# Kernel tuning notes

Hardware: AMD Instinct MI355X
Metric: run time of the kernel (lower is better)

The kernel has to match this reference:

```python
import jax, jax.numpy as jnp
import numpy as np

N = 50000      # nodes
E = 800000     # edges (before self-loops)
IN = 256       # in_channels
HID = 128      # hidden_channels
OUT = 128      # out_channels
NEG_SLOPE = 0.2
EPS = 1e-16


def setup_inputs() -> dict:
    key = jax.random.key(0)
    ks = jax.random.split(key, 16)
    p = lambda k, shape: jax.random.normal(k, shape, jnp.float32) * 0.1
    return {
        "x": jax.random.normal(ks[0], (N, IN), jnp.float32),
        "edge_index": jax.random.randint(ks[1], (2, E), 0, N, dtype=jnp.int64),
        # semantic MLP
        "W1": p(ks[2], (IN, HID)), "b1": jnp.zeros((HID,), jnp.float32),
        "W2": p(ks[3], (HID, HID)), "b2": jnp.zeros((HID,), jnp.float32),
        # gat1: HID -> HID//2, heads=4, concat -> 2*HID
        "g1_W": p(ks[4], (HID, 4 * (HID // 2))),
        "g1_as": p(ks[5], (4, HID // 2)), "g1_ad": p(ks[6], (4, HID // 2)),
        "g1_b": jnp.zeros((4 * (HID // 2),), jnp.float32),
        # gat2: 2*HID -> OUT, heads=2, mean -> OUT
        "g2_W": p(ks[7], (2 * HID, 2 * OUT)),
        "g2_as": p(ks[8], (2, OUT)), "g2_ad": p(ks[9], (2, OUT)),
        "g2_b": jnp.zeros((OUT,), jnp.float32),
        # gat3: OUT -> OUT, heads=1, mean -> OUT
        "g3_W": p(ks[10], (OUT, OUT)),
        "g3_as": p(ks[11], (1, OUT)), "g3_ad": p(ks[12], (1, OUT)),
        "g3_b": jnp.zeros((OUT,), jnp.float32),
    }


def _gat(h_in, src, dst, W, a_src, a_dst, bias, heads, concat, n):
    # Linear projection into heads: [n, H, C]
    h = (h_in @ W).reshape(n, heads, -1)
    alpha_s = jnp.sum(h * a_src[None], axis=-1)  # [n, H]
    alpha_d = jnp.sum(h * a_dst[None], axis=-1)  # [n, H]
    e = jax.nn.leaky_relu(alpha_s[src] + alpha_d[dst], NEG_SLOPE)  # [E', H]
    # segment softmax over edges grouped by destination node
    m = jax.ops.segment_max(e, dst, num_segments=n)
    ex = jnp.exp(e - m[dst])
    denom = jax.ops.segment_sum(ex, dst, num_segments=n)
    alpha = ex / (denom[dst] + EPS)  # [E', H]
    msg = h[src] * alpha[..., None]  # [E', H, C]
    out = jax.ops.segment_sum(msg, dst, num_segments=n)  # [n, H, C]
    out = out.reshape(n, -1) if concat else out.mean(axis=1)
    return out + bias


def reference(x, edge_index, W1, b1, W2, b2,
              g1_W, g1_as, g1_ad, g1_b,
              g2_W, g2_as, g2_ad, g2_b,
              g3_W, g3_as, g3_ad, g3_b):
    n = x.shape[0]
    # PyG GATConv add_self_loops=True: append self-loop edges once
    loops = jnp.arange(n, dtype=edge_index.dtype)
    src = jnp.concatenate([edge_index[0], loops])
    dst = jnp.concatenate([edge_index[1], loops])
    # semantic MLP (inference: dropout = identity)
    h = jax.nn.relu(x @ W1 + b1)
    h = jax.nn.relu(h @ W2 + b2)
    h = jax.nn.elu(_gat(h, src, dst, g1_W, g1_as, g1_ad, g1_b, 4, True, n))
    h = jax.nn.elu(_gat(h, src, dst, g2_W, g2_as, g2_ad, g2_b, 2, False, n))
    h = _gat(h, src, dst, g3_W, g3_as, g3_ad, g3_b, 1, False, n)
    return h
```

## Files before the change

kernel.cpp:

```cpp
#include <hip/hip_runtime.h>
#include <math.h>


#define NEG_SLOPE 0.2f
#define EPS_DEN 1e-16f

typedef __attribute__((ext_vector_type(8))) short short8;
typedef __attribute__((ext_vector_type(4))) float f32x4;
typedef __attribute__((ext_vector_type(2))) float f32x2;
typedef __attribute__((ext_vector_type(4))) unsigned short u16x4;

__device__ inline unsigned short f2b(float f) {
  unsigned u = __builtin_bit_cast(unsigned, f);
  unsigned r = (u + 0x7fffu + ((u >> 16) & 1u)) >> 16;
  return (unsigned short)r;
}
__device__ inline float b2f(unsigned short u) {
  return __builtin_bit_cast(float, (unsigned)u << 16);
}

__device__ inline void glds16(const void* g, void* l) {
  __builtin_amdgcn_global_load_lds(
      (const __attribute__((address_space(1))) void*)g,
      (__attribute__((address_space(3))) void*)l, 16, 0, 0);
}

__device__ inline f32x2 pk_fma(f32x2 a, f32x2 b, f32x2 c) {
  f32x2 d;
  asm("v_pk_fma_f32 %0, %1, %2, %3" : "=v"(d) : "v"(a), "v"(b), "v"(c));
  return d;
}

__device__ inline void accum8(f32x2 acc2[4], const short8 r, float w) {
  const f32x2 wv = {w, w};
  const unsigned* u = (const unsigned*)&r;
#pragma unroll
  for (int p = 0; p < 4; p++) {
    const unsigned lo = u[p] << 16;
    const unsigned hi = u[p] & 0xffff0000u;
    f32x2 val = {__builtin_bit_cast(float, lo), __builtin_bit_cast(float, hi)};
    acc2[p] = pk_fma(val, wv, acc2[p]);
  }
}

template <int H>
__device__ inline void loadH(const float* p, float* v) {
  if constexpr (H == 4) {
    float4 t = *(const float4*)p;
    v[0] = t.x; v[1] = t.y; v[2] = t.z; v[3] = t.w;
  } else if constexpr (H == 2) {
    float2 t = *(const float2*)p;
    v[0] = t.x; v[1] = t.y;
  } else {
    v[0] = *p;
  }
}

template <int ACT, int OBF, int H, int CC>
__global__ __launch_bounds__(256) void mfma_gemm(
    const unsigned short* __restrict__ A, const unsigned short* __restrict__ Bt,
    const float* __restrict__ bias, float* __restrict__ Cf,
    unsigned short* __restrict__ Cb, const float* __restrict__ a_s,
    const float* __restrict__ a_d, float* __restrict__ alS,
    float* __restrict__ alD, int n, int K, int M) {
  __shared__ unsigned short As[64 * 64];
  __shared__ unsigned short Bs[128 * 64];

  const int tid = threadIdx.x;
  const int w = tid >> 6, lane = tid & 63;
  const int row0 = blockIdx.x * 64, col0 = blockIdx.y * 128;
  const int lr = lane >> 3, lg = lane & 7;
  const int lm = lane & 15, kg = lane >> 4;
  const int wm = (w >> 1) * 32, wn = (w & 1) * 64;

  f32x4 acc[2][4];
#pragma unroll
  for (int i = 0; i < 2; i++)
#pragma unroll
    for (int j = 0; j < 4; j++) acc[i][j] = {0.f, 0.f, 0.f, 0.f};

  const int swz = (lg ^ lr) << 3;

  for (int k0 = 0; k0 < K; k0 += 64) {
    __syncthreads();
#pragma unroll
    for (int it = 0; it < 2; it++) {
      const int r = w * 16 + it * 8;
      glds16(A + (size_t)(row0 + r + lr) * K + k0 + swz, &As[r * 64]);
    }
#pragma unroll
    for (int it = 0; it < 4; it++) {
      const int r = w * 32 + it * 8;
      glds16(Bt + (size_t)(col0 + r + lr) * K + k0 + swz, &Bs[r * 64]);
    }
    __syncthreads();

#pragma unroll
    for (int kh = 0; kh < 2; kh++) {
      const int sw = ((kh * 4 + kg) ^ (lm & 7)) << 3;
      short8 aF[2], bF[4];
#pragma unroll
      for (int i = 0; i < 2; i++)
        aF[i] = *(const short8*)&As[(wm + i * 16 + lm) * 64 + sw];
#pragma unroll
      for (int j = 0; j < 4; j++)
        bF[j] = *(const short8*)&Bs[(wn + j * 16 + lm) * 64 + sw];
#pragma unroll
      for (int i = 0; i < 2; i++)
#pragma unroll
        for (int j = 0; j < 4; j++)
          acc[i][j] = __builtin_amdgcn_mfma_f32_16x16x32_bf16(
              aF[i], bF[j], acc[i][j], 0, 0, 0);
    }
  }

  const int r4 = kg * 4;

  if constexpr (H > 0) {
    const int head = (col0 + wn) / CC;
    const int ch0 = (col0 + wn) % CC;
    float asv[4], adv[4];
#pragma unroll
    for (int j = 0; j < 4; j++) {
      asv[j] = a_s[head * CC + ch0 + j * 16 + lm];
      adv[j] = a_d[head * CC + ch0 + j * 16 + lm];
    }
    float psA[2][4], pdA[2][4];
#pragma unroll
    for (int i = 0; i < 2; i++) {
#pragma unroll
      for (int r = 0; r < 4; r++) {
        float ps = 0.f, pd = 0.f;
#pragma unroll
        for (int j = 0; j < 4; j++) {
          ps += acc[i][j][r] * asv[j];
          pd += acc[i][j][r] * adv[j];
        }
#pragma unroll
        for (int off = 1; off < 16; off <<= 1) {
          ps += __shfl_xor(ps, off, 64);
          pd += __shfl_xor(pd, off, 64);
        }
        psA[i][r] = ps;
        pdA[i][r] = pd;
      }
    }
    if constexpr (CC == 64) {
      if (lm == 0) {
#pragma unroll
        for (int i = 0; i < 2; i++)
#pragma unroll
          for (int r = 0; r < 4; r++) {
            const int row = row0 + wm + i * 16 + r4 + r;
            if (row < n) {
              alS[(size_t)row * H + head] = psA[i][r];
              alD[(size_t)row * H + head] = pdA[i][r];
            }
          }
      }
    } else {
      __shared__ float redS[4][32];
      __shared__ float redD[4][32];
      if (lm == 0) {
#pragma unroll
        for (int i = 0; i < 2; i++)
#pragma unroll
          for (int r = 0; r < 4; r++) {
            redS[w][i * 16 + r4 + r] = psA[i][r];
            redD[w][i * 16 + r4 + r] = pdA[i][r];
          }
      }
      __syncthreads();
      if ((w & 1) == 0 && lane < 32) {
        const int row = row0 + wm + lane;
        if (row < n) {
          const int hd = col0 / CC;
          alS[(size_t)row * H + hd] = redS[w][lane] + redS[w + 1][lane];
          alD[(size_t)row * H + hd] = redD[w][lane] + redD[w + 1][lane];
        }
      }
    }
  }

#pragma unroll
  for (int j = 0; j < 4; j++) {
    const int col = col0 + wn + j * 16 + lm;
    const float bv = bias ? bias[col] : 0.f;
#pragma unroll
    for (int i = 0; i < 2; i++) {
#pragma unroll
      for (int r = 0; r < 4; r++) {
        const int row = row0 + wm + i * 16 + r4 + r;
        if (row < n) {
          float v = acc[i][j][r] + bv;
          if (ACT == 1) v = v > 0.f ? v : 0.f;
          if (OBF)
            Cb[(size_t)row * M + col] = f2b(v);
          else
            Cf[(size_t)row * M + col] = v;
        }
      }
    }
  }
}

__global__ __launch_bounds__(256) void mlp_g1_kernel(
    const unsigned short* __restrict__ X, const unsigned short* __restrict__ W1t,
    const float* __restrict__ b1, const unsigned short* __restrict__ W2t,
    const float* __restrict__ b2, const unsigned short* __restrict__ G1Wt,
    const float* __restrict__ a_s, const float* __restrict__ a_d,
    float* __restrict__ alS, float* __restrict__ alD,
    unsigned short* __restrict__ Pb,
    const int* __restrict__ esrc, const int* __restrict__ edst,
    const int* __restrict__ rank, const int* __restrict__ rowptr,
    int* __restrict__ csr_src, int E, int n) {
  __shared__ unsigned short As[64 * 64];
  __shared__ unsigned short Bs[128 * 64];
  __shared__ unsigned short H1s[64 * 136];

  const int tid = threadIdx.x;
  const int w = tid >> 6, lane = tid & 63;
  const int row0 = blockIdx.x * 64;
  const int lr = lane >> 3, lg = lane & 7;
  const int lm = lane & 15, kg = lane >> 4;
  const int wm = (w >> 1) * 32, wn = (w & 1) * 64;
  const int swz = (lg ^ lr) << 3;
  const int r4 = kg * 4;

  {
    const int tot = E + n;
    const int gsz = (int)gridDim.x * 256;
    for (int i = (int)blockIdx.x * 256 + tid; i < tot; i += gsz) {
      int s, d;
      if (i < E) {
        s = __builtin_nontemporal_load(esrc + i);
        d = __builtin_nontemporal_load(edst + i);
      } else {
        s = d = i - E;
      }
      if ((unsigned)d < (unsigned)n && (unsigned)s < (unsigned)n) {
        const int pos = rowptr[d] + __builtin_nontemporal_load(rank + i);
        __builtin_nontemporal_store(s, csr_src + pos);
      }
    }
  }

  f32x4 acc[2][4];
#pragma unroll
  for (int i = 0; i < 2; i++)
#pragma unroll
    for (int j = 0; j < 4; j++) acc[i][j] = {0.f, 0.f, 0.f, 0.f};

  for (int k0 = 0; k0 < 256; k0 += 64) {
    __syncthreads();
#pragma unroll
    for (int it = 0; it < 2; it++) {
      const int r = w * 16 + it * 8;
      glds16(X + (size_t)(row0 + r + lr) * 256 + k0 + swz, &As[r * 64]);
    }
#pragma unroll
    for (int it = 0; it < 4; it++) {
      const int r = w * 32 + it * 8;
      glds16(W1t + (size_t)(r + lr) * 256 + k0 + swz, &Bs[r * 64]);
    }
    __syncthreads();
#pragma unroll
    for (int kh = 0; kh < 2; kh++) {
      const int sw = ((kh * 4 + kg) ^ (lm & 7)) << 3;
      short8 aF[2], bF[4];
#pragma unroll
      for (int i = 0; i < 2; i++)
        aF[i] = *(const short8*)&As[(wm + i * 16 + lm) * 64 + sw];
#pragma unroll
      for (int j = 0; j < 4; j++)
        bF[j] = *(const short8*)&Bs[(wn + j * 16 + lm) * 64 + sw];
#pragma unroll
      for (int i = 0; i < 2; i++)
#pragma unroll
        for (int j = 0; j < 4; j++)
          acc[i][j] = __builtin_amdgcn_mfma_f32_16x16x32_bf16(
              aF[i], bF[j], acc[i][j], 0, 0, 0);
    }
  }

#pragma unroll
  for (int j = 0; j < 4; j++) {
    const int col = wn + j * 16 + lm;
    const float bv = b1[col];
#pragma unroll
    for (int i = 0; i < 2; i++) {
#pragma unroll
      for (int r = 0; r < 4; r++) {
        const int lrow = wm + i * 16 + r4 + r;
        float v = acc[i][j][r] + bv;
        v = v > 0.f ? v : 0.f;
        H1s[lrow * 136 + col] = f2b(v);
      }
    }
  }
#pragma unroll
  for (int i = 0; i < 2; i++)
#pragma unroll
    for (int j = 0; j < 4; j++) acc[i][j] = {0.f, 0.f, 0.f, 0.f};
  __syncthreads();

  for (int k0 = 0; k0 < 128; k0 += 64) {
    __syncthreads();
#pragma unroll
    for (int it = 0; it < 4; it++) {
      const int r = w * 32 + it * 8;
      glds16(W2t + (size_t)(r + lr) * 128 + k0 + swz, &Bs[r * 64]);
    }
    __syncthreads();
#pragma unroll
    for (int kh = 0; kh < 2; kh++) {
      const int swB = ((kh * 4 + kg) ^ (lm & 7)) << 3;
      const int kofs = k0 + (kh * 4 + kg) * 8;
      short8 aF[2], bF[4];
#pragma unroll
      for (int i = 0; i < 2; i++)
        aF[i] = *(const short8*)&H1s[(wm + i * 16 + lm) * 136 + kofs];
#pragma unroll
      for (int j = 0; j < 4; j++)
        bF[j] = *(const short8*)&Bs[(wn + j * 16 + lm) * 64 + swB];
#pragma unroll
      for (int i = 0; i < 2; i++)
#pragma unroll
        for (int j = 0; j < 4; j++)
          acc[i][j] = __builtin_amdgcn_mfma_f32_16x16x32_bf16(
              aF[i], bF[j], acc[i][j], 0, 0, 0);
    }
  }

  __syncthreads();
#pragma unroll
  for (int j = 0; j < 4; j++) {
    const int col = wn + j * 16 + lm;
    const float bv = b2[col];
#pragma unroll
    for (int i = 0; i < 2; i++) {
#pragma unroll
      for (int r = 0; r < 4; r++) {
        const int lrow = wm + i * 16 + r4 + r;
        float v = acc[i][j][r] + bv;
        v = v > 0.f ? v : 0.f;
        H1s[lrow * 136 + col] = f2b(v);
      }
    }
  }
  __syncthreads();

  for (int c = 0; c < 2; c++) {
#pragma unroll
    for (int i = 0; i < 2; i++)
#pragma unroll
      for (int j = 0; j < 4; j++) acc[i][j] = {0.f, 0.f, 0.f, 0.f};

    for (int k0 = 0; k0 < 128; k0 += 64) {
      __syncthreads();
#pragma unroll
      for (int it = 0; it < 4; it++) {
        const int r = w * 32 + it * 8;
        glds16(G1Wt + (size_t)(c * 128 + r + lr) * 128 + k0 + swz,
               &Bs[r * 64]);
      }
      __syncthreads();
#pragma unroll
      for (int kh = 0; kh < 2; kh++) {
        const int swB = ((kh * 4 + kg) ^ (lm & 7)) << 3;
        const int kofs = k0 + (kh * 4 + kg) * 8;
        short8 aF[2], bF[4];
#pragma unroll
        for (int i = 0; i < 2; i++)
          aF[i] = *(const short8*)&H1s[(wm + i * 16 + lm) * 136 + kofs];
#pragma unroll
        for (int j = 0; j < 4; j++)
          bF[j] = *(const short8*)&Bs[(wn + j * 16 + lm) * 64 + swB];
#pragma unroll
        for (int i = 0; i < 2; i++)
#pragma unroll
          for (int j = 0; j < 4; j++)
            acc[i][j] = __builtin_amdgcn_mfma_f32_16x16x32_bf16(
                aF[i], bF[j], acc[i][j], 0, 0, 0);
      }
    }

    {
      const int head = c * 2 + (wn >> 6);
      float asv[4], adv[4];
#pragma unroll
      for (int j = 0; j < 4; j++) {
        asv[j] = a_s[head * 64 + j * 16 + lm];
        adv[j] = a_d[head * 64 + j * 16 + lm];
      }
#pragma unroll
      for (int i = 0; i < 2; i++) {
#pragma unroll
        for (int r = 0; r < 4; r++) {
          float ps = 0.f, pd = 0.f;
#pragma unroll
          for (int j = 0; j < 4; j++) {
            ps += acc[i][j][r] * asv[j];
            pd += acc[i][j][r] * adv[j];
          }
#pragma unroll
          for (int off = 1; off < 16; off <<= 1) {
            ps += __shfl_xor(ps, off, 64);
            pd += __shfl_xor(pd, off, 64);
          }
          if (lm == 0) {
            const int row = row0 + wm + i * 16 + r4 + r;
            if (row < n) {
              alS[(size_t)row * 4 + head] = ps;
              alD[(size_t)row * 4 + head] = pd;
            }
          }
        }
      }
    }

#pragma unroll
    for (int j = 0; j < 4; j++) {
      const int col = c * 128 + wn + j * 16 + lm;
#pragma unroll
      for (int i = 0; i < 2; i++) {
#pragma unroll
        for (int r = 0; r < 4; r++) {
          const int row = row0 + wm + i * 16 + r4 + r;
          if (row < n) Pb[(size_t)row * 256 + col] = f2b(acc[i][j][r]);
        }
      }
    }
  }
}

struct PrepArgs {
  const float* x; unsigned short* xb; long long nx;
  const float* W[5]; unsigned short* Wt[5];
  int K[5], M[5], t0[6];
  int* deg; int* rank; const int* edst; int E; int N;
};

__global__ __launch_bounds__(256) void fused_prep_kernel(PrepArgs a) {
  const int tid = threadIdx.x, bid = blockIdx.x, nb = gridDim.x;
  const long long gt = (long long)bid * 256 + tid;
  const long long gsz = (long long)nb * 256;
  __shared__ float tt[32][33];

  const long long etot = (long long)a.E + a.N;
  for (long long i = gt; i < etot; i += gsz) {
    int d = (i < a.E) ? __builtin_nontemporal_load(a.edst + i)
                      : (int)(i - a.E);
    if ((unsigned)d < (unsigned)a.N)
      a.rank[i] = atomicAdd(&a.deg[d], 1);
  }
  for (long long i = gt * 4; i < a.nx; i += gsz * 4) {
    float4 v = *(const float4*)(a.x + i);
    u16x4 u = {f2b(v.x), f2b(v.y), f2b(v.z), f2b(v.w)};
    *(u16x4*)(a.xb + i) = u;
  }
  for (int t = bid; t < a.t0[5]; t += nb) {
    int di = 0;
    while (t >= a.t0[di + 1]) di++;
    const int local = t - a.t0[di];
    const int K = a.K[di], M = a.M[di], mtiles = M / 32;
    const int mb = (local % mtiles) * 32, kb = (local / mtiles) * 32;
    const float* W = a.W[di];
    unsigned short* Wt = a.Wt[di];
    const int tx = tid & 31, ty = tid >> 5;
    __syncthreads();
#pragma unroll
    for (int i = 0; i < 4; i++)
      tt[ty + i * 8][tx] = W[(size_t)(kb + ty + i * 8) * M + mb + tx];
    __syncthreads();
#pragma unroll
    for (int i = 0; i < 4; i++)
      Wt[(size_t)(mb + ty + i * 8) * K + kb + tx] = f2b(tt[tx][ty + i * 8]);
  }
}

__global__ __launch_bounds__(256) void block_reduce_kernel(
    const int* __restrict__ deg, int* __restrict__ bsum, int n) {
  __shared__ int s[256];
  const int t = threadIdx.x, i = blockIdx.x * 256 + t;
  s[t] = (i < n) ? deg[i] : 0;
  __syncthreads();
#pragma unroll
  for (int off = 128; off; off >>= 1) {
    if (t < off) s[t] += s[t + off];
    __syncthreads();
  }
  if (t == 0) bsum[blockIdx.x] = s[0];
}

__global__ __launch_bounds__(256) void scan_bsums_kernel(int* __restrict__ bsum,
                                                         int nb) {
  __shared__ int s[256];
  const int t = threadIdx.x;
  const int v = (t < nb) ? bsum[t] : 0;
  s[t] = v;
  __syncthreads();
#pragma unroll
  for (int off = 1; off < 256; off <<= 1) {
    int a = (t >= off) ? s[t - off] : 0;
    __syncthreads();
    s[t] += a;
    __syncthreads();
  }
  if (t < nb) bsum[t] = s[t] - v;
}

__global__ __launch_bounds__(256) void scan_final_kernel(
    const int* __restrict__ deg, const int* __restrict__ bsumx,
    int* __restrict__ rowptr, int n) {
  __shared__ int s[256];
  const int t = threadIdx.x, i = blockIdx.x * 256 + t;
  const int v = (i < n) ? deg[i] : 0;
  s[t] = v;
  __syncthreads();
#pragma unroll
  for (int off = 1; off < 256; off <<= 1) {
    int a = (t >= off) ? s[t - off] : 0;
    __syncthreads();
    s[t] += a;
    __syncthreads();
  }
  if (i < n) {
    const int base = bsumx[blockIdx.x];
    rowptr[i] = base + s[t] - v;
    if (i == n - 1) rowptr[n] = base + s[t];
  }
}

template <int H, int C, bool CONCAT, int ACT, int OBF>
__global__ __launch_bounds__(256) void gat_fused_kernel(
    const unsigned short* __restrict__ proj, const float* __restrict__ alpha_s,
    const float* __restrict__ alpha_d, const int* __restrict__ rowptr,
    const int* __restrict__ csr_src, const float* __restrict__ bias,
    void* __restrict__ out, int n) {
  constexpr int HC = H * C;
  constexpr int ROWSPAN = HC / 8;
  constexpr int EDGES = 64 / ROWSPAN;
  constexpr int WLANES = C / 8;

  __shared__ float exs[4][64 * H];
  __shared__ int sids[4][64];

  const int wv = threadIdx.x >> 6;
  const int wid = (blockIdx.x * blockDim.x + threadIdx.x) >> 6;
  const int lane = threadIdx.x & 63;
  if (wid >= n) return;
  const int dst = wid;
  const int eslot = lane / ROWSPAN;
  const int sl = lane % ROWSPAN;
  const int h_lane = (sl * 8) / C;
  float* myex = &exs[wv][0];
  int* mysid = &sids[wv][0];

  float adv[H];
  loadH<H>(alpha_d + (size_t)dst * H, adv);
  const int rs = rowptr[dst], re = rowptr[dst + 1];

  float denomp[H];
#pragma unroll
  for (int h = 0; h < H; h++) denomp[h] = 0.f;
  f32x2 acc2[4];
#pragma unroll
  for (int p = 0; p < 4; p++) acc2[p] = {0.f, 0.f};

  const unsigned short* prow = proj + sl * 8;

  for (int base = rs; base < re; base += 64) {
    const int cnt = min(64, re - base);
    if (lane < cnt) {
      const int s = __builtin_nontemporal_load(csr_src + base + lane);
      mysid[lane] = s;
      float as[H];
      loadH<H>(alpha_s + (size_t)s * H, as);
#pragma unroll
      for (int h = 0; h < H; h++) {
        float e = as[h] + adv[h];
        e = e > 0.f ? e : NEG_SLOPE * e;
        const float ex = __expf(e);
        denomp[h] += ex;
        myex[lane * H + h] = ex;
      }
    }
    __builtin_amdgcn_wave_barrier();
    int j = eslot;
    for (; j + EDGES < cnt; j += 2 * EDGES) {
      const int s0 = mysid[j];
      const int s1 = mysid[j + EDGES];
      const float w0 = myex[j * H + h_lane];
      const float w1 = myex[(j + EDGES) * H + h_lane];
      const short8 r0 = *(const short8*)(prow + (size_t)s0 * HC);
      const short8 r1 = *(const short8*)(prow + (size_t)s1 * HC);
      accum8(acc2, r0, w0);
      accum8(acc2, r1, w1);
    }
    for (; j < cnt; j += EDGES) {
      const int s0 = mysid[j];
      const float w0 = myex[j * H + h_lane];
      const short8 r0 = *(const short8*)(prow + (size_t)s0 * HC);
      accum8(acc2, r0, w0);
    }
    __builtin_amdgcn_wave_barrier();
  }

  float acc[8];
#pragma unroll
  for (int p = 0; p < 4; p++) {
    acc[2 * p] = acc2[p].x;
    acc[2 * p + 1] = acc2[p].y;
  }

#pragma unroll
  for (int off = 32; off; off >>= 1)
#pragma unroll
    for (int h = 0; h < H; h++)
      denomp[h] += __shfl_xor(denomp[h], off, 64);
#pragma unroll
  for (int off = ROWSPAN; off < 64; off <<= 1)
#pragma unroll
    for (int k = 0; k < 8; k++) acc[k] += __shfl_xor(acc[k], off, 64);

  const float inv = 1.f / (denomp[h_lane] + EPS_DEN);
  float v[8];
#pragma unroll
  for (int k = 0; k < 8; k++) v[k] = acc[k] * inv;

  if (!CONCAT && H == 2) {
#pragma unroll
    for (int k = 0; k < 8; k++) v[k] += __shfl_xor(v[k], 16, 64);
  }

  if (CONCAT) {
    if (eslot != 0) return;
    const int c0 = sl * 8;
    float vv[8];
#pragma unroll
    for (int k = 0; k < 8; k++) {
      float t = v[k] + bias[c0 + k];
      if (ACT == 1) t = t > 0.f ? t : (__expf(t) - 1.f);
      vv[k] = t;
    }
    if (OBF) {
      short8 o;
#pragma unroll
      for (int k = 0; k < 8; k++) o[k] = (short)f2b(vv[k]);
      __builtin_nontemporal_store(
          o, (short8*)((unsigned short*)out + (size_t)dst * HC + c0));
    } else {
      float* op = (float*)out + (size_t)dst * HC + c0;
      f32x4 o0 = {vv[0], vv[1], vv[2], vv[3]};
      f32x4 o1 = {vv[4], vv[5], vv[6], vv[7]};
      __builtin_nontemporal_store(o0, (f32x4*)op);
      __builtin_nontemporal_store(o1, (f32x4*)(op + 4));
    }
  } else {
    if (eslot != 0 || sl >= WLANES) return;
    const int c0 = sl * 8;
    const float invH = 1.f / (float)H;
    float vv[8];
#pragma unroll
    for (int k = 0; k < 8; k++) {
      float t = v[k] * invH + bias[c0 + k];
      if (ACT == 1) t = t > 0.f ? t : (__expf(t) - 1.f);
      vv[k] = t;
    }
    if (OBF) {
      short8 o;
#pragma unroll
      for (int k = 0; k < 8; k++) o[k] = (short)f2b(vv[k]);
      __builtin_nontemporal_store(
          o, (short8*)((unsigned short*)out + (size_t)dst * C + c0));
    } else {
      float* op = (float*)out + (size_t)dst * C + c0;
      f32x4 o0 = {vv[0], vv[1], vv[2], vv[3]};
      f32x4 o1 = {vv[4], vv[5], vv[6], vv[7]};
      __builtin_nontemporal_store(o0, (f32x4*)op);
      __builtin_nontemporal_store(o1, (f32x4*)(op + 4));
    }
  }
}

extern "C" void kernel_launch(void* const* d_in, const int* in_sizes, int n_in,
                              void* d_out, int out_size, void* d_ws,
                              size_t ws_size, hipStream_t stream) {
  const float* x    = (const float*)d_in[0];
  const int*   ei   = (const int*)d_in[1];
  const float* W1   = (const float*)d_in[2];
  const float* b1   = (const float*)d_in[3];
  const float* W2   = (const float*)d_in[4];
  const float* b2   = (const float*)d_in[5];
  const float* g1W  = (const float*)d_in[6];
  const float* g1as = (const float*)d_in[7];
  const float* g1ad = (const float*)d_in[8];
  const float* g1b  = (const float*)d_in[9];
  const float* g2W  = (const float*)d_in[10];
  const float* g2as = (const float*)d_in[11];
  const float* g2ad = (const float*)d_in[12];
  const float* g2b  = (const float*)d_in[13];
  const float* g3W  = (const float*)d_in[14];
  const float* g3as = (const float*)d_in[15];
  const float* g3ad = (const float*)d_in[16];
  const float* g3b  = (const float*)d_in[17];

  const int N = in_sizes[0] / 256;
  const int E = in_sizes[1] / 2;
  const int Etot = E + N;
  const int NT = (N + 127) / 128;
  const int NT64 = (N + 63) / 64;
  const int NP = NT * 128;
  const int NB = (N + 255) / 256;

  char* p = (char*)d_ws;
  unsigned short* Pb  = (unsigned short*)p; p += (size_t)NP * 256 * 2;
  unsigned short* xb  = (unsigned short*)p; p += (size_t)NP * 256 * 2;
  unsigned short* h2b = (unsigned short*)p; p += (size_t)NP * 128 * 2;
  unsigned short* W1t = (unsigned short*)p; p += (size_t)128 * 256 * 2;
  unsigned short* W2t = (unsigned short*)p; p += (size_t)128 * 128 * 2;
  unsigned short* g1Wt = (unsigned short*)p; p += (size_t)256 * 128 * 2;
  unsigned short* g2Wt = (unsigned short*)p; p += (size_t)256 * 256 * 2;
  unsigned short* g3Wt = (unsigned short*)p; p += (size_t)128 * 128 * 2;
  float* alB = (float*)p; p += (size_t)N * 14 * 4;
  float* alS1 = alB;
  float* alD1 = alB + (size_t)4 * N;
  float* alS2 = alB + (size_t)8 * N;
  float* alD2 = alB + (size_t)10 * N;
  float* alS3 = alB + (size_t)12 * N;
  float* alD3 = alB + (size_t)13 * N;
  int* deg    = (int*)p; p += (size_t)N * 4;
  int* rowptr = (int*)p; p += (size_t)(N + 1) * 4;
  int* bsum   = (int*)p; p += 256 * 4;
  int* rank   = (int*)p; p += (size_t)Etot * 4;
  int* csrsrc = (int*)p;

  const int* esrc = ei;
  const int* edst = ei + E;
  unsigned short* act1b = xb;
  unsigned short* act2b = h2b;

  hipMemsetAsync(deg, 0, (size_t)N * 4, stream);

  PrepArgs pa;
  pa.x = x; pa.xb = xb; pa.nx = (long long)N * 256;
  pa.W[0] = W1;  pa.Wt[0] = W1t;  pa.K[0] = 256; pa.M[0] = 128;
  pa.W[1] = W2;  pa.Wt[1] = W2t;  pa.K[1] = 128; pa.M[1] = 128;
  pa.W[2] = g1W; pa.Wt[2] = g1Wt; pa.K[2] = 128; pa.M[2] = 256;
  pa.W[3] = g2W; pa.Wt[3] = g2Wt; pa.K[3] = 256; pa.M[3] = 256;
  pa.W[4] = g3W; pa.Wt[4] = g3Wt; pa.K[4] = 128; pa.M[4] = 128;
  pa.t0[0] = 0;
  for (int i = 0; i < 5; i++)
    pa.t0[i + 1] = pa.t0[i] + (pa.K[i] / 32) * (pa.M[i] / 32);
  pa.deg = deg; pa.rank = rank; pa.edst = edst; pa.E = E; pa.N = N;
  fused_prep_kernel<<<2048, 256, 0, stream>>>(pa);

  block_reduce_kernel<<<NB, 256, 0, stream>>>(deg, bsum, N);
  scan_bsums_kernel<<<1, 256, 0, stream>>>(bsum, NB);
  scan_final_kernel<<<NB, 256, 0, stream>>>(deg, bsum, rowptr, N);

  mlp_g1_kernel<<<NT64, 256, 0, stream>>>(xb, W1t, b1, W2t, b2, g1Wt, g1as,
                                          g1ad, alS1, alD1, Pb, esrc, edst,
                                          rank, rowptr, csrsrc, E, N);

  gat_fused_kernel<4, 64, true, 1, 1><<<(N + 3) / 4, 256, 0, stream>>>(
      Pb, alS1, alD1, rowptr, csrsrc, g1b, act1b, N);

  mfma_gemm<0, 1, 2, 128><<<dim3(NT64, 2), 256, 0, stream>>>(
      act1b, g2Wt, nullptr, nullptr, Pb, g2as, g2ad, alS2, alD2, N, 256, 256);
  gat_fused_kernel<2, 128, false, 1, 1><<<(N + 3) / 4, 256, 0, stream>>>(
      Pb, alS2, alD2, rowptr, csrsrc, g2b, act2b, N);

  mfma_gemm<0, 1, 1, 128><<<dim3(NT64, 1), 256, 0, stream>>>(
      act2b, g3Wt, nullptr, nullptr, Pb, g3as, g3ad, alS3, alD3, N, 128, 128);
  gat_fused_kernel<1, 128, false, 0, 0><<<(N + 3) / 4, 256, 0, stream>>>(
      Pb, alS3, alD3, rowptr, csrsrc, g3b, d_out, N);
}
```

Baseline: 423.2 us.

## Build CSR degree counts with LDS-privatized per-chunk histograms instead of global atomics

Replaces the global atomicAdd degree counting in the prep kernel with a separate kernel that splits edges into 32 chunks and nodes into 16 ranges, counting in shared-memory histograms. Per-chunk counts are summed for degrees and turned into per-chunk prefix offsets that the CSR scatter adds to each edge's position. This targets contention on global atomics, at the cost of rereading the edge list once per node range, a 32×N histogram buffer, and an extra launch plus longer reduce and scan passes.

```diff
diff --git a/kernel.cpp b/kernel.cpp
--- a/kernel.cpp
+++ b/kernel.cpp
@@ -4,6 +4,8 @@
 
 #define NEG_SLOPE 0.2f
 #define EPS_DEN 1e-16f
+#define PR 16
+#define QC 32
 
 typedef __attribute__((ext_vector_type(8))) short short8;
 typedef __attribute__((ext_vector_type(4))) float f32x4;
@@ -213,7 +215,7 @@
     unsigned short* __restrict__ Pb,
     const int* __restrict__ esrc, const int* __restrict__ edst,
     const int* __restrict__ rank, const int* __restrict__ rowptr,
-    int* __restrict__ csr_src, int E, int n) {
+    const int* __restrict__ Cpref, int* __restrict__ csr_src, int E, int n) {
   __shared__ unsigned short As[64 * 64];
   __shared__ unsigned short Bs[128 * 64];
   __shared__ unsigned short H1s[64 * 136];
@@ -229,6 +231,7 @@
 
   {
     const int tot = E + n;
+    const int CS = (tot + QC - 1) / QC;
     const int gsz = (int)gridDim.x * 256;
     for (int i = (int)blockIdx.x * 256 + tid; i < tot; i += gsz) {
       int s, d;
@@ -239,7 +242,9 @@
         s = d = i - E;
       }
       if ((unsigned)d < (unsigned)n && (unsigned)s < (unsigned)n) {
-        const int pos = rowptr[d] + __builtin_nontemporal_load(rank + i);
+        const int q = i / CS;
+        const int pos = rowptr[d] + Cpref[(size_t)q * n + d] +
+                        __builtin_nontemporal_load(rank + i);
         __builtin_nontemporal_store(s, csr_src + pos);
       }
     }
@@ -438,7 +443,6 @@
   const float* x; unsigned short* xb; long long nx;
   const float* W[5]; unsigned short* Wt[5];
   int K[5], M[5], t0[6];
-  int* deg; int* rank; const int* edst; int E; int N;
 };
 
 __global__ __launch_bounds__(256) void fused_prep_kernel(PrepArgs a) {
@@ -447,13 +451,6 @@
   const long long gsz = (long long)nb * 256;
   __shared__ float tt[32][33];
 
-  const long long etot = (long long)a.E + a.N;
-  for (long long i = gt; i < etot; i += gsz) {
-    int d = (i < a.E) ? __builtin_nontemporal_load(a.edst + i)
-                      : (int)(i - a.E);
-    if ((unsigned)d < (unsigned)a.N)
-      a.rank[i] = atomicAdd(&a.deg[d], 1);
-  }
   for (long long i = gt * 4; i < a.nx; i += gsz * 4) {
     float4 v = *(const float4*)(a.x + i);
     u16x4 u = {f2b(v.x), f2b(v.y), f2b(v.z), f2b(v.w)};
@@ -479,11 +476,46 @@
   }
 }
 
+__global__ __launch_bounds__(256) void count_hist_kernel(
+    const int* __restrict__ edst, int* __restrict__ rank,
+    int* __restrict__ C, int E, int n) {
+  __shared__ int h[3200];
+  const int tid = threadIdx.x;
+  const int q = blockIdx.x, p = blockIdx.y;
+  const int RANGE = (n + PR - 1) / PR;
+  const int lo = p * RANGE;
+
+  for (int i = tid; i < RANGE; i += 256) h[i] = 0;
+  __syncthreads();
+
+  const int tot = E + n;
+  const int CS = (tot + QC - 1) / QC;
+  const int start = q * CS;
+  const int end = min(start + CS, tot);
+  for (int i = start + tid; i < end; i += 256) {
+    int d = (i < E) ? __builtin_nontemporal_load(edst + i) : (i - E);
+    const int r = d - lo;
+    if ((unsigned)r < (unsigned)RANGE && d < n)
+      __builtin_nontemporal_store(atomicAdd(&h[r], 1), rank + i);
+  }
+  __syncthreads();
+
+  for (int i = tid; i < RANGE; i += 256)
+    if (lo + i < n) C[(size_t)q * n + lo + i] = h[i];
+}
+
 __global__ __launch_bounds__(256) void block_reduce_kernel(
-    const int* __restrict__ deg, int* __restrict__ bsum, int n) {
+    const int* __restrict__ C, int* __restrict__ deg, int* __restrict__ bsum,
+    int n) {
   __shared__ int s[256];
   const int t = threadIdx.x, i = blockIdx.x * 256 + t;
-  s[t] = (i < n) ? deg[i] : 0;
+  int v = 0;
+  if (i < n) {
+#pragma unroll
+    for (int q = 0; q < QC; q++) v += C[(size_t)q * n + i];
+    deg[i] = v;
+  }
+  s[t] = v;
   __syncthreads();
 #pragma unroll
   for (int off = 128; off; off >>= 1) {
@@ -511,8 +543,8 @@
 }
 
 __global__ __launch_bounds__(256) void scan_final_kernel(
-    const int* __restrict__ deg, const int* __restrict__ bsumx,
-    int* __restrict__ rowptr, int n) {
+    const int* __restrict__ deg, int* __restrict__ C,
+    const int* __restrict__ bsumx, int* __restrict__ rowptr, int n) {
   __shared__ int s[256];
   const int t = threadIdx.x, i = blockIdx.x * 256 + t;
   const int v = (i < n) ? deg[i] : 0;
@@ -529,6 +561,13 @@
     const int base = bsumx[blockIdx.x];
     rowptr[i] = base + s[t] - v;
     if (i == n - 1) rowptr[n] = base + s[t];
+    int run = 0;
+#pragma unroll
+    for (int q = 0; q < QC; q++) {
+      const int c = C[(size_t)q * n + i];
+      C[(size_t)q * n + i] = run;
+      run += c;
+    }
   }
 }
 
@@ -734,6 +773,7 @@
   int* rowptr = (int*)p; p += (size_t)(N + 1) * 4;
   int* bsum   = (int*)p; p += 256 * 4;
   int* rank   = (int*)p; p += (size_t)Etot * 4;
+  int* Chist  = (int*)p; p += (size_t)QC * N * 4;
   int* csrsrc = (int*)p;
 
   const int* esrc = ei;
@@ -741,7 +781,7 @@
   unsigned short* act1b = xb;
   unsigned short* act2b = h2b;
 
-  hipMemsetAsync(deg, 0, (size_t)N * 4, stream);
+  count_hist_kernel<<<dim3(QC, PR), 256, 0, stream>>>(edst, rank, Chist, E, N);
 
   PrepArgs pa;
   pa.x = x; pa.xb = xb; pa.nx = (long long)N * 256;
@@ -753,16 +793,15 @@
   pa.t0[0] = 0;
   for (int i = 0; i < 5; i++)
     pa.t0[i + 1] = pa.t0[i] + (pa.K[i] / 32) * (pa.M[i] / 32);
-  pa.deg = deg; pa.rank = rank; pa.edst = edst; pa.E = E; pa.N = N;
   fused_prep_kernel<<<2048, 256, 0, stream>>>(pa);
 
-  block_reduce_kernel<<<NB, 256, 0, stream>>>(deg, bsum, N);
+  block_reduce_kernel<<<NB, 256, 0, stream>>>(Chist, deg, bsum, N);
   scan_bsums_kernel<<<1, 256, 0, stream>>>(bsum, NB);
-  scan_final_kernel<<<NB, 256, 0, stream>>>(deg, bsum, rowptr, N);
+  scan_final_kernel<<<NB, 256, 0, stream>>>(deg, Chist, bsum, rowptr, N);
 
   mlp_g1_kernel<<<NT64, 256, 0, stream>>>(xb, W1t, b1, W2t, b2, g1Wt, g1as,
                                           g1ad, alS1, alD1, Pb, esrc, edst,
-                                          rank, rowptr, csrsrc, E, N);
+                                          rank, rowptr, Chist, csrsrc, E, N);
 
   gat_fused_kernel<4, 64, true, 1, 1><<<(N + 3) / 4, 256, 0, stream>>>(
       Pb, alS1, alD1, rowptr, csrsrc, g1b, act1b, N);
```

After: 453.2 us. +7.1%, slower.
